# Kernel optimization log

Measured on AMD Instinct MI355X. Metric: run time of the kernel, lower is better.

Reference implementation:

```python
import jax, jax.numpy as jnp
import numpy as np

EPS = 1e-12  # torch F.normalize default eps


def _l2_normalize(t):
    n = jnp.linalg.norm(t, axis=-1, keepdims=True)
    return t / jnp.maximum(n, EPS)


def _block(x, W, alpha):
    # x: [B,H,N,D]; W: [D,D] (torch Linear weight, applied as x @ W.T)
    xn = _l2_normalize(x)                                   # q_norm == k_norm (q=k=x)
    A = jnp.einsum('bhnd,bhmd->bhnm', xn, xn)               # cosine similarity [B,H,N,N]
    A = jax.nn.softmax(A / jnp.maximum(alpha, 0.01), axis=-1)
    av = jnp.einsum('bhnm,bhmd->bhnd', A, x)                # A @ v, v = x
    return jax.nn.relu(jnp.einsum('bhnd,ed->bhne', av, W) + x)


def setup_inputs() -> dict:
    key = jax.random.key(0)
    k1, k2, k3 = jax.random.split(key, 3)
    B, H, N, D = 4, 4, 4096, 64
    x = jax.random.normal(k1, (B, H, N, D), dtype=jnp.float32)
    # nn.Linear(dim, dim, bias=False) weights, kaiming-uniform-ish scale
    bound = 1.0 / np.sqrt(D)
    W1 = jax.random.uniform(k2, (D, D), dtype=jnp.float32, minval=-bound, maxval=bound)
    W2 = jax.random.uniform(k3, (D, D), dtype=jnp.float32, minval=-bound, maxval=bound)
    alpha1 = jnp.float32(1.0)
    alpha2 = jnp.float32(1.0)
    return {"x": x, "W1": W1, "W2": W2, "alpha1": alpha1, "alpha2": alpha2}


def reference(x, W1, W2, alpha1, alpha2):
    x = _block(x, W1, alpha1)
    x = _block(x, W2, alpha2)
    return x
```

## Files before the change

### kernel.cpp

```cpp
#include <hip/hip_runtime.h>

typedef unsigned short u16;
typedef unsigned int   u32;
typedef __bf16 bf16x8 __attribute__((ext_vector_type(8)));
typedef float  f32x16 __attribute__((ext_vector_type(16)));

#define BH    16
#define NSEQ  4096
#define DIM   64
#define BM    128
#define BN    64
#define LDP   72
#define NTH   32
#define QTILES (NSEQ / BM)

#define SK_OFF   0
#define SV_OFF   9216
#define SW_OFF   18432
#define LX_OFF   23040
#define SMEM_U16 23552
#define HBUF     4608

#define MFMA __builtin_amdgcn_mfma_f32_32x32x16_bf16

__device__ __forceinline__ float bf2f(u16 u) {
    union { u32 i; float f; } v; v.i = ((u32)u) << 16; return v.f;
}
__device__ __forceinline__ u16 f2bf(float f) {
    union { float f; u32 i; } v; v.f = f;
    u32 r = v.i + 0x7fffu + ((v.i >> 16) & 1u);
    return (u16)(r >> 16);
}
#if __has_builtin(__builtin_amdgcn_exp2f)
__device__ __forceinline__ float exp2_raw(float x) { return __builtin_amdgcn_exp2f(x); }
#else
__device__ __forceinline__ float exp2_raw(float x) {
    float r; asm("v_exp_f32 %0, %1" : "=v"(r) : "v"(x)); return r;
}
#endif
__device__ __forceinline__ u32 cvtpk(float a, float b) {
    u32 r; asm("v_cvt_pk_bf16_f32 %0, %1, %2" : "=v"(r) : "v"(a), "v"(b)); return r;
}
__device__ __forceinline__ void plswap(u32& a, u32& b) {
    asm("v_permlane32_swap_b32 %0, %1" : "+v"(a), "+v"(b));
}
__device__ __forceinline__ void lds_barrier() {
    asm volatile("s_waitcnt lgkmcnt(0)\n\ts_barrier" ::: "memory");
}

__global__ __launch_bounds__(256) void ContentGCN_5059471475267_prepn(
    const float* __restrict__ src, u16* __restrict__ xn)
{
    int gid = blockIdx.x * 256 + threadIdx.x;
    int row = gid >> 2, cg = (gid & 3) * 16;
    size_t base = (size_t)row * DIM + cg;

    float v[16];
    const float4* g = (const float4*)(src + base);
#pragma unroll
    for (int i = 0; i < 4; i++) {
        float4 t = g[i];
        v[4*i] = t.x; v[4*i+1] = t.y; v[4*i+2] = t.z; v[4*i+3] = t.w;
    }
    float ss = 0.f;
#pragma unroll
    for (int d = 0; d < 16; d++) ss += v[d] * v[d];
    ss += __shfl_xor(ss, 1);
    ss += __shfl_xor(ss, 2);
    float n = sqrtf(ss);
    if (n < 1e-12f) n = 1e-12f;
    float inv = 1.0f / n;

    alignas(16) u16 nb[16];
#pragma unroll
    for (int d = 0; d < 16; d++) nb[d] = f2bf(v[d] * inv);
    uint4* gn = (uint4*)(xn + base);
    gn[0] = ((uint4*)nb)[0]; gn[1] = ((uint4*)nb)[1];
}

__global__ __launch_bounds__(256) void ContentGCN_5059471475267_preptr(
    const void* __restrict__ src, int isf, u16* __restrict__ xT)
{
    __shared__ u16 tile[16 * 264];
    int bh = blockIdx.x >> 6, nt = (blockIdx.x >> 2) & 15, dq = blockIdx.x & 3;
    int r = threadIdx.x;
    size_t sbase = ((size_t)bh * NSEQ + nt * 256 + r) * DIM + dq * 16;

    u16 vals[16];
    if (isf) {
        const float4* g = (const float4*)((const float*)src + sbase);
#pragma unroll
        for (int i = 0; i < 4; i++) {
            float4 t = g[i];
            vals[4*i]   = f2bf(t.x); vals[4*i+1] = f2bf(t.y);
            vals[4*i+2] = f2bf(t.z); vals[4*i+3] = f2bf(t.w);
        }
    } else {
        alignas(16) u16 tmp[16];
        const uint4* g = (const uint4*)((const u16*)src + sbase);
        ((uint4*)tmp)[0] = g[0]; ((uint4*)tmp)[1] = g[1];
#pragma unroll
        for (int d = 0; d < 16; d++) vals[d] = tmp[d];
    }
#pragma unroll
    for (int d = 0; d < 16; d++) tile[d * 264 + r] = vals[d];
    __syncthreads();

    int d = threadIdx.x >> 4, nch = threadIdx.x & 15;
    uint4 o0 = *(const uint4*)&tile[d * 264 + nch * 16];
    uint4 o1 = *(const uint4*)&tile[d * 264 + nch * 16 + 8];
    size_t tb = ((size_t)bh * DIM + dq * 16 + d) * NSEQ + (size_t)nt * 256 + nch * 16;
    *(uint4*)&xT[tb]     = o0;
    *(uint4*)&xT[tb + 8] = o1;
}

__global__ __launch_bounds__(512, 4) void ContentGCN_5059471475267_attn(
    const u16* __restrict__ xn, const u16* __restrict__ xT,
    const void* __restrict__ res, int res_isf,
    const float* __restrict__ Wt, const float* __restrict__ alphap,
    void* __restrict__ outp, int out_isf, u16* __restrict__ xnout)
{
    __shared__ u16 smem[SMEM_U16];
    u16* sK = smem + SK_OFF;
    u16* sV = smem + SV_OFF;
    u16* sW = smem + SW_OFF;
    float* lX = (float*)(smem + LX_OFF);

    int tid  = threadIdx.x;
    int w    = tid >> 6, lane = tid & 63;
    int half = w >> 2,  wv   = w & 3;
    int l31  = lane & 31, hi = lane >> 5;
    int bh   = blockIdx.x >> 5;
    int qt   = blockIdx.x & 31;

    float scale = 1.4426950408889634f / fmaxf(alphap[0], 0.01f);

    {
        int rr = tid >> 3, c0 = (tid & 7) * 8;
        const float4* gw = (const float4*)(Wt + rr * DIM + c0);
        float4 t0 = gw[0], t1 = gw[1];
        alignas(16) u16 wb[8];
        wb[0] = f2bf(t0.x); wb[1] = f2bf(t0.y); wb[2] = f2bf(t0.z); wb[3] = f2bf(t0.w);
        wb[4] = f2bf(t1.x); wb[5] = f2bf(t1.y); wb[6] = f2bf(t1.z); wb[7] = f2bf(t1.w);
        *(uint4*)&sW[rr * LDP + c0] = *(const uint4*)wb;
    }

    int qrow = qt * BM + wv * 32 + l31;
    const u16* qp = xn + ((size_t)bh * NSEQ + qrow) * DIM + hi * 8;
    bf16x8 bQ0 = *(const bf16x8*)(qp);
    bf16x8 bQ1 = *(const bf16x8*)(qp + 16);
    bf16x8 bQ2 = *(const bf16x8*)(qp + 32);
    bf16x8 bQ3 = *(const bf16x8*)(qp + 48);

    f32x16 z16;
#pragma unroll
    for (int i = 0; i < 16; i++) z16[i] = 0.f;
    f32x16 OT0 = z16, OT1 = z16;
    float la0 = 0.f, la1 = 0.f, la2 = 0.f, la3 = 0.f;

    u16* sKh = sK + half * HBUF;
    u16* sVh = sV + half * HBUF;

    int ltid = tid & 255;
    int srow = ltid >> 2, scol = (ltid & 3) * 16;

    const u16* pk = xn + ((size_t)bh * NSEQ + half * (NTH * BN) + srow) * DIM + scol;
    const u16* pv = xT + ((size_t)bh * DIM + srow) * NSEQ + half * (NTH * BN) + scol;
    uint4 ck0 = ((const uint4*)pk)[0], ck1 = ((const uint4*)pk)[1];
    uint4 cv0 = ((const uint4*)pv)[0], cv1 = ((const uint4*)pv)[1];
    pk += (size_t)BN * DIM; pv += BN;

    const u16* kB  = sKh + l31 * LDP + hi * 8;
    const u16* vB0 = sVh + l31 * LDP + hi * 8;
    const u16* vB1 = sVh + (32 + l31) * LDP + hi * 8;

    for (int kt = 0; kt < NTH; kt++) {
        lds_barrier();
        *(uint4*)&sKh[srow * LDP + scol]     = ck0;
        *(uint4*)&sKh[srow * LDP + scol + 8] = ck1;
        *(uint4*)&sVh[srow * LDP + scol]     = cv0;
        *(uint4*)&sVh[srow * LDP + scol + 8] = cv1;
        if (kt + 1 < NTH) {
            ck0 = ((const uint4*)pk)[0]; ck1 = ((const uint4*)pk)[1];
            cv0 = ((const uint4*)pv)[0]; cv1 = ((const uint4*)pv)[1];
            pk += (size_t)BN * DIM; pv += BN;
        }
        lds_barrier();

        const u16* kb1 = kB + 32 * LDP;
        f32x16 ST0, ST1;
        __builtin_amdgcn_s_setprio(1);
        ST0 = MFMA(*(const bf16x8*)(kB),       bQ0, z16, 0, 0, 0);
        ST0 = MFMA(*(const bf16x8*)(kB + 16),  bQ1, ST0, 0, 0, 0);
        ST0 = MFMA(*(const bf16x8*)(kB + 32),  bQ2, ST0, 0, 0, 0);
        ST0 = MFMA(*(const bf16x8*)(kB + 48),  bQ3, ST0, 0, 0, 0);
        ST1 = MFMA(*(const bf16x8*)(kb1),      bQ0, z16, 0, 0, 0);
        ST1 = MFMA(*(const bf16x8*)(kb1 + 16), bQ1, ST1, 0, 0, 0);
        ST1 = MFMA(*(const bf16x8*)(kb1 + 32), bQ2, ST1, 0, 0, 0);
        ST1 = MFMA(*(const bf16x8*)(kb1 + 48), bQ3, ST1, 0, 0, 0);
        __builtin_amdgcn_s_setprio(0);

        {
            float p0  = exp2_raw(fmaf(ST0[0],  scale, -scale));
            float p1  = exp2_raw(fmaf(ST0[1],  scale, -scale));
            float p2  = exp2_raw(fmaf(ST0[2],  scale, -scale));
            float p3  = exp2_raw(fmaf(ST0[3],  scale, -scale));
            float p4  = exp2_raw(fmaf(ST0[4],  scale, -scale));
            float p5  = exp2_raw(fmaf(ST0[5],  scale, -scale));
            float p6  = exp2_raw(fmaf(ST0[6],  scale, -scale));
            float p7  = exp2_raw(fmaf(ST0[7],  scale, -scale));
            float p8  = exp2_raw(fmaf(ST0[8],  scale, -scale));
            float p9  = exp2_raw(fmaf(ST0[9],  scale, -scale));
            float p10 = exp2_raw(fmaf(ST0[10], scale, -scale));
            float p11 = exp2_raw(fmaf(ST0[11], scale, -scale));
            float p12 = exp2_raw(fmaf(ST0[12], scale, -scale));
            float p13 = exp2_raw(fmaf(ST0[13], scale, -scale));
            float p14 = exp2_raw(fmaf(ST0[14], scale, -scale));
            float p15 = exp2_raw(fmaf(ST0[15], scale, -scale));
            u32 w0 = cvtpk(p0,  p1),  w1 = cvtpk(p2,  p3);
            u32 w2 = cvtpk(p4,  p5),  w3 = cvtpk(p6,  p7);
            u32 w4 = cvtpk(p8,  p9),  w5 = cvtpk(p10, p11);
            u32 w6 = cvtpk(p12, p13), w7 = cvtpk(p14, p15);
            plswap(w0, w2); plswap(w1, w3);
            plswap(w4, w6); plswap(w5, w7);
            union { u32 u[4]; bf16x8 v; } bp0, bp1;
            bp0.u[0] = w0; bp0.u[1] = w1; bp0.u[2] = w2; bp0.u[3] = w3;
            bp1.u[0] = w4; bp1.u[1] = w5; bp1.u[2] = w6; bp1.u[3] = w7;
            __builtin_amdgcn_s_setprio(1);
            OT0 = MFMA(*(const bf16x8*)(vB0),      bp0.v, OT0, 0, 0, 0);
            OT0 = MFMA(*(const bf16x8*)(vB0 + 16), bp1.v, OT0, 0, 0, 0);
            OT1 = MFMA(*(const bf16x8*)(vB1),      bp0.v, OT1, 0, 0, 0);
            OT1 = MFMA(*(const bf16x8*)(vB1 + 16), bp1.v, OT1, 0, 0, 0);
            __builtin_amdgcn_s_setprio(0);
            la0 += (p0 + p4) + (p8  + p12);
            la1 += (p1 + p5) + (p9  + p13);
            la2 += (p2 + p6) + (p10 + p14);
            la3 += (p3 + p7) + (p11 + p15);
        }

        {
            float p0  = exp2_raw(fmaf(ST1[0],  scale, -scale));
            float p1  = exp2_raw(fmaf(ST1[1],  scale, -scale));
            float p2  = exp2_raw(fmaf(ST1[2],  scale, -scale));
            float p3  = exp2_raw(fmaf(ST1[3],  scale, -scale));
            float p4  = exp2_raw(fmaf(ST1[4],  scale, -scale));
            float p5  = exp2_raw(fmaf(ST1[5],  scale, -scale));
            float p6  = exp2_raw(fmaf(ST1[6],  scale, -scale));
            float p7  = exp2_raw(fmaf(ST1[7],  scale, -scale));
            float p8  = exp2_raw(fmaf(ST1[8],  scale, -scale));
            float p9  = exp2_raw(fmaf(ST1[9],  scale, -scale));
            float p10 = exp2_raw(fmaf(ST1[10], scale, -scale));
            float p11 = exp2_raw(fmaf(ST1[11], scale, -scale));
            float p12 = exp2_raw(fmaf(ST1[12], scale, -scale));
            float p13 = exp2_raw(fmaf(ST1[13], scale, -scale));
            float p14 = exp2_raw(fmaf(ST1[14], scale, -scale));
            float p15 = exp2_raw(fmaf(ST1[15], scale, -scale));
            u32 w0 = cvtpk(p0,  p1),  w1 = cvtpk(p2,  p3);
            u32 w2 = cvtpk(p4,  p5),  w3 = cvtpk(p6,  p7);
            u32 w4 = cvtpk(p8,  p9),  w5 = cvtpk(p10, p11);
            u32 w6 = cvtpk(p12, p13), w7 = cvtpk(p14, p15);
            plswap(w0, w2); plswap(w1, w3);
            plswap(w4, w6); plswap(w5, w7);
            union { u32 u[4]; bf16x8 v; } bp0, bp1;
            bp0.u[0] = w0; bp0.u[1] = w1; bp0.u[2] = w2; bp0.u[3] = w3;
            bp1.u[0] = w4; bp1.u[1] = w5; bp1.u[2] = w6; bp1.u[3] = w7;
            __builtin_amdgcn_s_setprio(1);
            OT0 = MFMA(*(const bf16x8*)(vB0 + 32), bp0.v, OT0, 0, 0, 0);
            OT0 = MFMA(*(const bf16x8*)(vB0 + 48), bp1.v, OT0, 0, 0, 0);
            OT1 = MFMA(*(const bf16x8*)(vB1 + 32), bp0.v, OT1, 0, 0, 0);
            OT1 = MFMA(*(const bf16x8*)(vB1 + 48), bp1.v, OT1, 0, 0, 0);
            __builtin_amdgcn_s_setprio(0);
            la0 += (p0 + p4) + (p8  + p12);
            la1 += (p1 + p5) + (p9  + p13);
            la2 += (p2 + p6) + (p10 + p14);
            la3 += (p3 + p7) + (p11 + p15);
        }
    }

    float lsum = (la0 + la1) + (la2 + la3);
    u32 ja = __float_as_uint(lsum), jb = ja;
    plswap(ja, jb);
    float lfull = __uint_as_float(ja) + __uint_as_float(jb);

    __syncthreads();
    if (lane < 32) lX[w * 32 + l31] = lfull;
    __syncthreads();
    float invl = 1.0f / (lfull + lX[(w ^ 4) * 32 + l31]);

    union { u32 u[4]; bf16x8 v; } av0, av1, av2, av3;
    {
        u32 x0 = cvtpk(OT0[0]  * invl, OT0[1]  * invl), x1 = cvtpk(OT0[2]  * invl, OT0[3]  * invl);
        u32 x2 = cvtpk(OT0[4]  * invl, OT0[5]  * invl), x3 = cvtpk(OT0[6]  * invl, OT0[7]  * invl);
        u32 x4 = cvtpk(OT0[8]  * invl, OT0[9]  * invl), x5 = cvtpk(OT0[10] * invl, OT0[11] * invl);
        u32 x6 = cvtpk(OT0[12] * invl, OT0[13] * invl), x7 = cvtpk(OT0[14] * invl, OT0[15] * invl);
        plswap(x0, x2); plswap(x1, x3); plswap(x4, x6); plswap(x5, x7);
        av0.u[0] = x0; av0.u[1] = x1; av0.u[2] = x2; av0.u[3] = x3;
        av1.u[0] = x4; av1.u[1] = x5; av1.u[2] = x6; av1.u[3] = x7;
        u32 y0 = cvtpk(OT1[0]  * invl, OT1[1]  * invl), y1 = cvtpk(OT1[2]  * invl, OT1[3]  * invl);
        u32 y2 = cvtpk(OT1[4]  * invl, OT1[5]  * invl), y3 = cvtpk(OT1[6]  * invl, OT1[7]  * invl);
        u32 y4 = cvtpk(OT1[8]  * invl, OT1[9]  * invl), y5 = cvtpk(OT1[10] * invl, OT1[11] * invl);
        u32 y6 = cvtpk(OT1[12] * invl, OT1[13] * invl), y7 = cvtpk(OT1[14] * invl, OT1[15] * invl);
        plswap(y0, y2); plswap(y1, y3); plswap(y4, y6); plswap(y5, y7);
        av2.u[0] = y0; av2.u[1] = y1; av2.u[2] = y2; av2.u[3] = y3;
        av3.u[0] = y4; av3.u[1] = y5; av3.u[2] = y6; av3.u[3] = y7;
    }

    f32x16 R0, R1;
    {
        const u16* w0p = sW + l31 * LDP + hi * 8;
        const u16* w1p = sW + (32 + l31) * LDP + hi * 8;
        R0 = MFMA(*(const bf16x8*)(w0p),      av0.v, z16, 0, 0, 0);
        R0 = MFMA(*(const bf16x8*)(w0p + 16), av1.v, R0,  0, 0, 0);
        R0 = MFMA(*(const bf16x8*)(w0p + 32), av2.v, R0,  0, 0, 0);
        R0 = MFMA(*(const bf16x8*)(w0p + 48), av3.v, R0,  0, 0, 0);
        R1 = MFMA(*(const bf16x8*)(w1p),      av0.v, z16, 0, 0, 0);
        R1 = MFMA(*(const bf16x8*)(w1p + 16), av1.v, R1,  0, 0, 0);
        R1 = MFMA(*(const bf16x8*)(w1p + 32), av2.v, R1,  0, 0, 0);
        R1 = MFMA(*(const bf16x8*)(w1p + 48), av3.v, R1,  0, 0, 0);
    }

    float* outS = (float*)smem;
    if (half == 0) {
#pragma unroll
        for (int r = 0; r < 16; r++) {
            int e0 = (r & 3) + 8 * (r >> 2) + 4 * hi;
            outS[e0 * 133 + wv * 32 + l31]        = R0[r];
            outS[(e0 + 32) * 133 + wv * 32 + l31] = R1[r];
        }
    }
    __syncthreads();
    if (half == 1) {
#pragma unroll
        for (int r = 0; r < 16; r++) {
            int e0 = (r & 3) + 8 * (r >> 2) + 4 * hi;
            outS[e0 * 133 + wv * 32 + l31]        += R0[r];
            outS[(e0 + 32) * 133 + wv * 32 + l31] += R1[r];
        }
    }
    __syncthreads();

    {
        int q = tid >> 2, c = tid & 3;
        size_t gbase = ((size_t)bh * NSEQ + qt * BM + q) * DIM + c * 16;
        float vv[16];
#pragma unroll
        for (int j = 0; j < 16; j++) vv[j] = outS[(c * 16 + j) * 133 + q];
        if (res_isf) {
            const float4* rp = (const float4*)((const float*)res + gbase);
#pragma unroll
            for (int i = 0; i < 4; i++) {
                float4 t = rp[i];
                vv[4*i] += t.x; vv[4*i+1] += t.y; vv[4*i+2] += t.z; vv[4*i+3] += t.w;
            }
        } else {
            alignas(16) u16 rb[16];
            const uint4* rp = (const uint4*)((const u16*)res + gbase);
            ((uint4*)rb)[0] = rp[0]; ((uint4*)rb)[1] = rp[1];
#pragma unroll
            for (int j = 0; j < 16; j++) vv[j] += bf2f(rb[j]);
        }
#pragma unroll
        for (int j = 0; j < 16; j++) vv[j] = (vv[j] < 0.f) ? 0.f : vv[j];
        if (out_isf) {
            float4* op = (float4*)((float*)outp + gbase);
#pragma unroll
            for (int i = 0; i < 4; i++)
                op[i] = make_float4(vv[4*i], vv[4*i+1], vv[4*i+2], vv[4*i+3]);
        } else {
            alignas(16) u16 ob[16];
#pragma unroll
            for (int j = 0; j < 16; j++) ob[j] = f2bf(vv[j]);
            uint4* op = (uint4*)((u16*)outp + gbase);
            op[0] = ((uint4*)ob)[0]; op[1] = ((uint4*)ob)[1];
        }
        if (xnout) {
            float ss = 0.f;
#pragma unroll
            for (int j = 0; j < 16; j++) ss += vv[j] * vv[j];
            ss += __shfl_xor(ss, 1);
            ss += __shfl_xor(ss, 2);
            float n = sqrtf(ss);
            if (n < 1e-12f) n = 1e-12f;
            float inv = 1.0f / n;
            alignas(16) u16 nb[16];
#pragma unroll
            for (int j = 0; j < 16; j++) nb[j] = f2bf(vv[j] * inv);
            uint4* gn = (uint4*)(xnout + gbase);
            gn[0] = ((uint4*)nb)[0]; gn[1] = ((uint4*)nb)[1];
        }
    }
}

extern "C" void kernel_launch(void* const* d_in, const int* in_sizes, int n_in,
                              void* d_out, int out_size, void* d_ws, size_t ws_size,
                              hipStream_t stream) {
    const float* x  = (const float*)d_in[0];
    const float* W1 = (const float*)d_in[1];
    const float* W2 = (const float*)d_in[2];
    const float* a1 = (const float*)d_in[3];
    const float* a2 = (const float*)d_in[4];
    float* outp = (float*)d_out;

    size_t elems = (size_t)BH * NSEQ * DIM;
    u16* xn1 = (u16*)d_ws;
    u16* xT  = xn1 + elems;
    u16* xn2 = xT + elems;
    u16* y1  = xn2 + elems;

    dim3 pgrid(1024), pblk(256);
    dim3 agrid(BH * QTILES), ablk(512);

    ContentGCN_5059471475267_prepn<<<pgrid, pblk, 0, stream>>>(x, xn1);
    ContentGCN_5059471475267_preptr<<<pgrid, pblk, 0, stream>>>(x, 1, xT);
    ContentGCN_5059471475267_attn<<<agrid, ablk, 0, stream>>>(
        xn1, xT, x, 1, W1, a1, y1, 0, xn2);
    ContentGCN_5059471475267_preptr<<<pgrid, pblk, 0, stream>>>(y1, 0, xT);
    ContentGCN_5059471475267_attn<<<agrid, ablk, 0, stream>>>(
        xn2, xT, y1, 0, W2, a2, outp, 1, nullptr);
}
```

Before: 246.6 us.

## Fuse V transpose into attention kernel and fold softmax scale into Q

Drops the separate transpose kernels. The attention kernel now reads row-major V (the bf16 copy of x, or y1 directly) and transposes it while storing to LDS, using 2-byte scattered writes with a rotation swizzle to limit bank conflicts. The softmax scale is folded into the Q fragments at load time, which removes the per-element FMA before exp2 and also drops the constant max subtraction. This saves two launches and the global round trip for xT, at the cost of more LDS write instructions per tile. It also risks exp overflow for very small alpha and adds bf16 rounding of the scaled Q.

New measurement: 239.0 us, median of 2. -3.1%, faster.

```diff
diff --git a/kernel.cpp b/kernel.cpp
--- a/kernel.cpp
+++ b/kernel.cpp
@@ -47,9 +47,16 @@
 __device__ __forceinline__ void lds_barrier() {
     asm volatile("s_waitcnt lgkmcnt(0)\n\ts_barrier" ::: "memory");
 }
+__device__ __forceinline__ bf16x8 ldq_scaled(const u16* p, float s) {
+    union { u32 u[4]; bf16x8 v; } r;
+#pragma unroll
+    for (int i = 0; i < 4; i++)
+        r.u[i] = cvtpk(bf2f(p[2*i]) * s, bf2f(p[2*i+1]) * s);
+    return r.v;
+}
 
 __global__ __launch_bounds__(256) void ContentGCN_5059471475267_prepn(
-    const float* __restrict__ src, u16* __restrict__ xn)
+    const float* __restrict__ src, u16* __restrict__ xn, u16* __restrict__ xr)
 {
     int gid = blockIdx.x * 256 + threadIdx.x;
     int row = gid >> 2, cg = (gid & 3) * 16;
@@ -71,51 +78,17 @@
     if (n < 1e-12f) n = 1e-12f;
     float inv = 1.0f / n;
 
-    alignas(16) u16 nb[16];
-#pragma unroll
-    for (int d = 0; d < 16; d++) nb[d] = f2bf(v[d] * inv);
+    alignas(16) u16 nb[16], rb[16];
+#pragma unroll
+    for (int d = 0; d < 16; d++) { nb[d] = f2bf(v[d] * inv); rb[d] = f2bf(v[d]); }
     uint4* gn = (uint4*)(xn + base);
     gn[0] = ((uint4*)nb)[0]; gn[1] = ((uint4*)nb)[1];
-}
-
-__global__ __launch_bounds__(256) void ContentGCN_5059471475267_preptr(
-    const void* __restrict__ src, int isf, u16* __restrict__ xT)
-{
-    __shared__ u16 tile[16 * 264];
-    int bh = blockIdx.x >> 6, nt = (blockIdx.x >> 2) & 15, dq = blockIdx.x & 3;
-    int r = threadIdx.x;
-    size_t sbase = ((size_t)bh * NSEQ + nt * 256 + r) * DIM + dq * 16;
-
-    u16 vals[16];
-    if (isf) {
-        const float4* g = (const float4*)((const float*)src + sbase);
-#pragma unroll
-        for (int i = 0; i < 4; i++) {
-            float4 t = g[i];
-            vals[4*i]   = f2bf(t.x); vals[4*i+1] = f2bf(t.y);
-            vals[4*i+2] = f2bf(t.z); vals[4*i+3] = f2bf(t.w);
-        }
-    } else {
-        alignas(16) u16 tmp[16];
-        const uint4* g = (const uint4*)((const u16*)src + sbase);
-        ((uint4*)tmp)[0] = g[0]; ((uint4*)tmp)[1] = g[1];
-#pragma unroll
-        for (int d = 0; d < 16; d++) vals[d] = tmp[d];
-    }
-#pragma unroll
-    for (int d = 0; d < 16; d++) tile[d * 264 + r] = vals[d];
-    __syncthreads();
-
-    int d = threadIdx.x >> 4, nch = threadIdx.x & 15;
-    uint4 o0 = *(const uint4*)&tile[d * 264 + nch * 16];
-    uint4 o1 = *(const uint4*)&tile[d * 264 + nch * 16 + 8];
-    size_t tb = ((size_t)bh * DIM + dq * 16 + d) * NSEQ + (size_t)nt * 256 + nch * 16;
-    *(uint4*)&xT[tb]     = o0;
-    *(uint4*)&xT[tb + 8] = o1;
+    uint4* gr = (uint4*)(xr + base);
+    gr[0] = ((uint4*)rb)[0]; gr[1] = ((uint4*)rb)[1];
 }
 
 __global__ __launch_bounds__(512, 4) void ContentGCN_5059471475267_attn(
-    const u16* __restrict__ xn, const u16* __restrict__ xT,
+    const u16* __restrict__ xn, const u16* __restrict__ vsrc,
     const void* __restrict__ res, int res_isf,
     const float* __restrict__ Wt, const float* __restrict__ alphap,
     void* __restrict__ outp, int out_isf, u16* __restrict__ xnout)
@@ -147,10 +120,10 @@
 
     int qrow = qt * BM + wv * 32 + l31;
     const u16* qp = xn + ((size_t)bh * NSEQ + qrow) * DIM + hi * 8;
-    bf16x8 bQ0 = *(const bf16x8*)(qp);
-    bf16x8 bQ1 = *(const bf16x8*)(qp + 16);
-    bf16x8 bQ2 = *(const bf16x8*)(qp + 32);
-    bf16x8 bQ3 = *(const bf16x8*)(qp + 48);
+    bf16x8 bQ0 = ldq_scaled(qp,      scale);
+    bf16x8 bQ1 = ldq_scaled(qp + 16, scale);
+    bf16x8 bQ2 = ldq_scaled(qp + 32, scale);
+    bf16x8 bQ3 = ldq_scaled(qp + 48, scale);
 
     f32x16 z16;
 #pragma unroll
@@ -163,27 +136,38 @@
 
     int ltid = tid & 255;
     int srow = ltid >> 2, scol = (ltid & 3) * 16;
-
-    const u16* pk = xn + ((size_t)bh * NSEQ + half * (NTH * BN) + srow) * DIM + scol;
-    const u16* pv = xT + ((size_t)bh * DIM + srow) * NSEQ + half * (NTH * BN) + scol;
+    int nl   = (srow + ((ltid & 3) << 4)) & 63;
+
+    const u16* pk = xn   + ((size_t)bh * NSEQ + half * (NTH * BN) + srow) * DIM + scol;
+    const u16* pv = vsrc + ((size_t)bh * NSEQ + half * (NTH * BN) + srow) * DIM + scol;
     uint4 ck0 = ((const uint4*)pk)[0], ck1 = ((const uint4*)pk)[1];
     uint4 cv0 = ((const uint4*)pv)[0], cv1 = ((const uint4*)pv)[1];
-    pk += (size_t)BN * DIM; pv += BN;
-
-    const u16* kB  = sKh + l31 * LDP + hi * 8;
-    const u16* vB0 = sVh + l31 * LDP + hi * 8;
-    const u16* vB1 = sVh + (32 + l31) * LDP + hi * 8;
+    pk += (size_t)BN * DIM; pv += (size_t)BN * DIM;
+
+    const u16* kB = sKh + l31 * LDP + hi * 8;
+
+    int g  = l31 >> 4;
+    int r0 = ((g)     & 3) << 4;
+    int r1 = ((g + 1) & 3) << 4;
+    int r2 = ((g + 2) & 3) << 4;
+    int r3 = ((g + 3) & 3) << 4;
+    const u16* vA = sVh + l31 * LDP + hi * 8;
+    const u16* vB = sVh + (32 + l31) * LDP + hi * 8;
 
     for (int kt = 0; kt < NTH; kt++) {
         lds_barrier();
         *(uint4*)&sKh[srow * LDP + scol]     = ck0;
         *(uint4*)&sKh[srow * LDP + scol + 8] = ck1;
-        *(uint4*)&sVh[srow * LDP + scol]     = cv0;
-        *(uint4*)&sVh[srow * LDP + scol + 8] = cv1;
+        {
+            alignas(16) u16 vb[16];
+            ((uint4*)vb)[0] = cv0; ((uint4*)vb)[1] = cv1;
+#pragma unroll
+            for (int j = 0; j < 16; j++) sVh[(scol + j) * LDP + nl] = vb[j];
+        }
         if (kt + 1 < NTH) {
             ck0 = ((const uint4*)pk)[0]; ck1 = ((const uint4*)pk)[1];
             cv0 = ((const uint4*)pv)[0]; cv1 = ((const uint4*)pv)[1];
-            pk += (size_t)BN * DIM; pv += BN;
+            pk += (size_t)BN * DIM; pv += (size_t)BN * DIM;
         }
         lds_barrier();
 
@@ -201,22 +185,22 @@
         __builtin_amdgcn_s_setprio(0);
 
         {
-            float p0  = exp2_raw(fmaf(ST0[0],  scale, -scale));
-            float p1  = exp2_raw(fmaf(ST0[1],  scale, -scale));
-            float p2  = exp2_raw(fmaf(ST0[2],  scale, -scale));
-            float p3  = exp2_raw(fmaf(ST0[3],  scale, -scale));
-            float p4  = exp2_raw(fmaf(ST0[4],  scale, -scale));
-            float p5  = exp2_raw(fmaf(ST0[5],  scale, -scale));
-            float p6  = exp2_raw(fmaf(ST0[6],  scale, -scale));
-            float p7  = exp2_raw(fmaf(ST0[7],  scale, -scale));
-            float p8  = exp2_raw(fmaf(ST0[8],  scale, -scale));
-            float p9  = exp2_raw(fmaf(ST0[9],  scale, -scale));
-            float p10 = exp2_raw(fmaf(ST0[10], scale, -scale));
-            float p11 = exp2_raw(fmaf(ST0[11], scale, -scale));
-            float p12 = exp2_raw(fmaf(ST0[12], scale, -scale));
-            float p13 = exp2_raw(fmaf(ST0[13], scale, -scale));
-            float p14 = exp2_raw(fmaf(ST0[14], scale, -scale));
-            float p15 = exp2_raw(fmaf(ST0[15], scale, -scale));
+            float p0  = exp2_raw(ST0[0]);
+            float p1  = exp2_raw(ST0[1]);
+            float p2  = exp2_raw(ST0[2]);
+            float p3  = exp2_raw(ST0[3]);
+            float p4  = exp2_raw(ST0[4]);
+            float p5  = exp2_raw(ST0[5]);
+            float p6  = exp2_raw(ST0[6]);
+            float p7  = exp2_raw(ST0[7]);
+            float p8  = exp2_raw(ST0[8]);
+            float p9  = exp2_raw(ST0[9]);
+            float p10 = exp2_raw(ST0[10]);
+            float p11 = exp2_raw(ST0[11]);
+            float p12 = exp2_raw(ST0[12]);
+            float p13 = exp2_raw(ST0[13]);
+            float p14 = exp2_raw(ST0[14]);
+            float p15 = exp2_raw(ST0[15]);
             u32 w0 = cvtpk(p0,  p1),  w1 = cvtpk(p2,  p3);
             u32 w2 = cvtpk(p4,  p5),  w3 = cvtpk(p6,  p7);
             u32 w4 = cvtpk(p8,  p9),  w5 = cvtpk(p10, p11);
@@ -227,10 +211,10 @@
             bp0.u[0] = w0; bp0.u[1] = w1; bp0.u[2] = w2; bp0.u[3] = w3;
             bp1.u[0] = w4; bp1.u[1] = w5; bp1.u[2] = w6; bp1.u[3] = w7;
             __builtin_amdgcn_s_setprio(1);
-            OT0 = MFMA(*(const bf16x8*)(vB0),      bp0.v, OT0, 0, 0, 0);
-            OT0 = MFMA(*(const bf16x8*)(vB0 + 16), bp1.v, OT0, 0, 0, 0);
-            OT1 = MFMA(*(const bf16x8*)(vB1),      bp0.v, OT1, 0, 0, 0);
-            OT1 = MFMA(*(const bf16x8*)(vB1 + 16), bp1.v, OT1, 0, 0, 0);
+            OT0 = MFMA(*(const bf16x8*)(vA + r0), bp0.v, OT0, 0, 0, 0);
+            OT0 = MFMA(*(const bf16x8*)(vA + r1), bp1.v, OT0, 0, 0, 0);
+            OT1 = MFMA(*(const bf16x8*)(vB + r2), bp0.v, OT1, 0, 0, 0);
+            OT1 = MFMA(*(const bf16x8*)(vB + r3), bp1.v, OT1, 0, 0, 0);
             __builtin_amdgcn_s_setprio(0);
             la0 += (p0 + p4) + (p8  + p12);
             la1 += (p1 + p5) + (p9  + p13);
@@ -239,22 +223,22 @@
         }
 
         {
-            float p0  = exp2_raw(fmaf(ST1[0],  scale, -scale));
-            float p1  = exp2_raw(fmaf(ST1[1],  scale, -scale));
-            float p2  = exp2_raw(fmaf(ST1[2],  scale, -scale));
-            float p3  = exp2_raw(fmaf(ST1[3],  scale, -scale));
-            float p4  = exp2_raw(fmaf(ST1[4],  scale, -scale));
-            float p5  = exp2_raw(fmaf(ST1[5],  scale, -scale));
-            float p6  = exp2_raw(fmaf(ST1[6],  scale, -scale));
-            float p7  = exp2_raw(fmaf(ST1[7],  scale, -scale));
-            float p8  = exp2_raw(fmaf(ST1[8],  scale, -scale));
-            float p9  = exp2_raw(fmaf(ST1[9],  scale, -scale));
-            float p10 = exp2_raw(fmaf(ST1[10], scale, -scale));
-            float p11 = exp2_raw(fmaf(ST1[11], scale, -scale));
-            float p12 = exp2_raw(fmaf(ST1[12], scale, -scale));
-            float p13 = exp2_raw(fmaf(ST1[13], scale, -scale));
-            float p14 = exp2_raw(fmaf(ST1[14], scale, -scale));
-            float p15 = exp2_raw(fmaf(ST1[15], scale, -scale));
+            float p0  = exp2_raw(ST1[0]);
+            float p1  = exp2_raw(ST1[1]);
+            float p2  = exp2_raw(ST1[2]);
+            float p3  = exp2_raw(ST1[3]);
+            float p4  = exp2_raw(ST1[4]);
+            float p5  = exp2_raw(ST1[5]);
+            float p6  = exp2_raw(ST1[6]);
+            float p7  = exp2_raw(ST1[7]);
+            float p8  = exp2_raw(ST1[8]);
+            float p9  = exp2_raw(ST1[9]);
+            float p10 = exp2_raw(ST1[10]);
+            float p11 = exp2_raw(ST1[11]);
+            float p12 = exp2_raw(ST1[12]);
+            float p13 = exp2_raw(ST1[13]);
+            float p14 = exp2_raw(ST1[14]);
+            float p15 = exp2_raw(ST1[15]);
             u32 w0 = cvtpk(p0,  p1),  w1 = cvtpk(p2,  p3);
             u32 w2 = cvtpk(p4,  p5),  w3 = cvtpk(p6,  p7);
             u32 w4 = cvtpk(p8,  p9),  w5 = cvtpk(p10, p11);
@@ -265,10 +249,10 @@
             bp0.u[0] = w0; bp0.u[1] = w1; bp0.u[2] = w2; bp0.u[3] = w3;
             bp1.u[0] = w4; bp1.u[1] = w5; bp1.u[2] = w6; bp1.u[3] = w7;
             __builtin_amdgcn_s_setprio(1);
-            OT0 = MFMA(*(const bf16x8*)(vB0 + 32), bp0.v, OT0, 0, 0, 0);
-            OT0 = MFMA(*(const bf16x8*)(vB0 + 48), bp1.v, OT0, 0, 0, 0);
-            OT1 = MFMA(*(const bf16x8*)(vB1 + 32), bp0.v, OT1, 0, 0, 0);
-            OT1 = MFMA(*(const bf16x8*)(vB1 + 48), bp1.v, OT1, 0, 0, 0);
+            OT0 = MFMA(*(const bf16x8*)(vA + r2), bp0.v, OT0, 0, 0, 0);
+            OT0 = MFMA(*(const bf16x8*)(vA + r3), bp1.v, OT0, 0, 0, 0);
+            OT1 = MFMA(*(const bf16x8*)(vB + r0), bp0.v, OT1, 0, 0, 0);
+            OT1 = MFMA(*(const bf16x8*)(vB + r1), bp1.v, OT1, 0, 0, 0);
             __builtin_amdgcn_s_setprio(0);
             la0 += (p0 + p4) + (p8  + p12);
             la1 += (p1 + p5) + (p9  + p13);
@@ -403,18 +387,16 @@
 
     size_t elems = (size_t)BH * NSEQ * DIM;
     u16* xn1 = (u16*)d_ws;
-    u16* xT  = xn1 + elems;
-    u16* xn2 = xT + elems;
+    u16* xr  = xn1 + elems;
+    u16* xn2 = xr + elems;
     u16* y1  = xn2 + elems;
 
     dim3 pgrid(1024), pblk(256);
     dim3 agrid(BH * QTILES), ablk(512);
 
-    ContentGCN_5059471475267_prepn<<<pgrid, pblk, 0, stream>>>(x, xn1);
-    ContentGCN_5059471475267_preptr<<<pgrid, pblk, 0, stream>>>(x, 1, xT);
+    ContentGCN_5059471475267_prepn<<<pgrid, pblk, 0, stream>>>(x, xn1, xr);
     ContentGCN_5059471475267_attn<<<agrid, ablk, 0, stream>>>(
-        xn1, xT, x, 1, W1, a1, y1, 0, xn2);
-    ContentGCN_5059471475267_preptr<<<pgrid, pblk, 0, stream>>>(y1, 0, xT);
+        xn1, xr, x, 1, W1, a1, y1, 0, xn2);
     ContentGCN_5059471475267_attn<<<agrid, ablk, 0, stream>>>(
-        xn2, xT, y1, 0, W2, a2, outp, 1, nullptr);
-}
+        xn2, y1, y1, 0, W2, a2, outp, 1, nullptr);
+}
```
